# Performance work log

Hardware: AMD Instinct MI355X
Metric: run time of the kernel (lower is better)

The kernel has to match this reference:

```python
import jax, jax.numpy as jnp
from jax import lax
import numpy as np

RADIUS = 0.1
NSAMPLE = 32
STRIDE = 3
ED_NSAMPLE = 10


def _sqdist(a, b):
    # a: [B,M,3], b: [B,N,3] -> [B,M,N] squared euclidean distance
    return (jnp.sum(a * a, -1)[:, :, None] + jnp.sum(b * b, -1)[:, None, :]
            - 2.0 * jnp.einsum('bmc,bnc->bmn', a, b))


def setup_inputs() -> dict:
    key = jax.random.key(0)
    ks = jax.random.split(key, 16)
    B, N = 8, 4096
    s = 0.05
    inp = {
        'data': jax.random.normal(ks[0], (B, N, 3), dtype=jnp.float32),
        'numpoints': N,
        # stem MLP 3 -> 64
        'W_stem': jax.random.normal(ks[1], (3, 64), dtype=jnp.float32) * s,
        'b_stem': jnp.zeros((64,), jnp.float32),
        # SA shared MLP (3 dp + 64 fj) -> 128
        'W_sa': jax.random.normal(ks[2], (67, 128), dtype=jnp.float32) * s,
        'b_sa': jnp.zeros((128,), jnp.float32),
        # FP MLP (128 interp + 64 skip) -> 64
        'W_fp': jax.random.normal(ks[3], (192, 64), dtype=jnp.float32) * s,
        'b_fp': jnp.zeros((64,), jnp.float32),
        # eigen-feature MLP 3 -> 4 -> 4
        'W_e1': jax.random.normal(ks[4], (3, 4), dtype=jnp.float32) * s,
        'b_e1': jnp.zeros((4,), jnp.float32),
        'W_e2': jax.random.normal(ks[5], (4, 4), dtype=jnp.float32) * s,
        'b_e2': jnp.zeros((4,), jnp.float32),
        # conv_final 1x1: 68 -> 64, + BN affine
        'W_fin': jax.random.normal(ks[6], (68, 64), dtype=jnp.float32) * s,
        'b_fin': jnp.zeros((64,), jnp.float32),
        'gamma': jnp.ones((64,), jnp.float32),
        'beta': jnp.zeros((64,), jnp.float32),
    }
    return inp


def reference(data, numpoints, W_stem, b_stem, W_sa, b_sa, W_fp, b_fp,
              W_e1, b_e1, W_e2, b_e2, W_fin, b_fin, gamma, beta):
    B, N, _ = data.shape
    b_ix = jnp.arange(B)[:, None, None]

    # ---------- encoder: stem MLP ----------
    f0 = jax.nn.relu(data @ W_stem + b_stem)  # [B,N,64]

    # set abstraction: stride-subsample centers, ball query, dp_fj, MLP, max
    sub_idx = jnp.arange(0, N, STRIDE)
    new_xyz = data[:, sub_idx]                 # [B,M,3]
    d2 = _sqdist(new_xyz, data)                # [B,M,N]
    col = jnp.arange(N, dtype=jnp.int32)
    valid = d2 < RADIUS * RADIUS
    keys = jnp.where(valid, col, N + col)      # first-valid ball query ordering
    negk, _ = lax.top_k(-keys, NSAMPLE)
    idx = -negk                                # [B,M,ns]
    first = idx[..., :1]                       # self point always valid
    idx = jnp.where(idx >= N, first, idx)
    g_xyz = data[b_ix, idx]                    # [B,M,ns,3]
    dp = (g_xyz - new_xyz[:, :, None, :]) / RADIUS  # normalize_dp
    g_f = f0[b_ix, idx]                        # [B,M,ns,64]
    feat = jnp.concatenate([dp, g_f], -1)      # [B,M,ns,67]
    h = jax.nn.relu(feat @ W_sa + b_sa)        # [B,M,ns,128]
    f_sub = jnp.max(h, axis=2)                 # [B,M,128]

    # ---------- decoder: 3-NN inverse-distance feature propagation ----------
    d2f = _sqdist(data, new_xyz)               # [B,N,M]
    negd, nn = lax.top_k(-d2f, 3)
    w = 1.0 / (-negd + 1e-8)
    w = w / jnp.sum(w, -1, keepdims=True)      # [B,N,3]
    nbr_f = f_sub[b_ix, nn]                    # [B,N,3,128]
    interp = jnp.einsum('bnk,bnkc->bnc', w, nbr_f)
    f = jax.nn.relu(jnp.concatenate([interp, f0], -1) @ W_fp + b_fp)  # [B,N,64]

    # ---------- KNN covariance eigen-features ----------
    d2e = _sqdist(data, data)                  # [B,N,N]
    _, gidx = lax.top_k(-d2e, ED_NSAMPLE)      # [B,N,k]
    nbr = data[b_ix, gidx]                     # [B,N,k,3]
    cen = nbr - jnp.mean(nbr, axis=2, keepdims=True)
    cov = jnp.einsum('bnkc,bnkd->bncd', cen, cen) / ED_NSAMPLE  # [B,N,3,3]
    eig = jnp.linalg.eigvalsh(cov)             # [B,N,3] ascending
    ef = jax.nn.relu(eig @ W_e1 + b_e1) @ W_e2 + b_e2  # [B,N,4]

    # ---------- fused 1x1 conv + BN (training-mode stats) + relu ----------
    z_in = jnp.concatenate([f, ef], -1)        # [B,N,68]
    zc = z_in @ W_fin + b_fin                  # [B,N,64]
    mu = jnp.mean(zc, axis=(0, 1))
    var = jnp.var(zc, axis=(0, 1))
    z = jax.nn.relu((zc - mu) * lax.rsqrt(var + 1e-5) * gamma + beta)
    z = jnp.transpose(z, (0, 2, 1))            # [B,64,N]
    return (data, z)
```

## Files before the change

kernel.cpp:

```cpp
#include <hip/hip_runtime.h>
#include <stdint.h>

#define BB 8
#define NN 4096
#define MM 1366
#define NS 32
#define RAD2 0.01f
#define NCH 16
#define CHUNK (NN/NCH)

static_assert(NCH * CHUNK == NN, "chunking");

__device__ __forceinline__ float rl(float v, int l) {
    return __int_as_float(__builtin_amdgcn_readlane(__float_as_int(v), l));
}
__device__ __forceinline__ uint32_t um(uint32_t a, uint32_t b) { return a < b ? a : b; }
__device__ __forceinline__ uint32_t ux(uint32_t a, uint32_t b) { return a > b ? a : b; }
__device__ __forceinline__ uint32_t um3(uint32_t a, uint32_t b, uint32_t c) { return um(um(a, b), c); }

__device__ __forceinline__ void mrg2(uint32_t* kk, uint32_t s0, uint32_t s1) {
    uint32_t n0 = um(kk[0], s0);
    uint32_t n1 = um3(kk[1], ux(kk[0], s0), s1);
    uint32_t n2 = um3(kk[2], ux(kk[1], s0), ux(kk[0], s1));
    uint32_t n3 = um3(kk[3], ux(kk[2], s0), ux(kk[1], s1));
    uint32_t n4 = um3(kk[4], ux(kk[3], s0), ux(kk[2], s1));
    uint32_t n5 = um3(kk[5], ux(kk[4], s0), ux(kk[3], s1));
    uint32_t n6 = um3(kk[6], ux(kk[5], s0), ux(kk[4], s1));
    uint32_t n7 = um3(kk[7], ux(kk[6], s0), ux(kk[5], s1));
    uint32_t n8 = um3(kk[8], ux(kk[7], s0), ux(kk[6], s1));
    uint32_t n9 = um3(kk[9], ux(kk[8], s0), ux(kk[7], s1));
    kk[0]=n0; kk[1]=n1; kk[2]=n2; kk[3]=n3; kk[4]=n4;
    kk[5]=n5; kk[6]=n6; kk[7]=n7; kk[8]=n8; kk[9]=n9;
}

__device__ __forceinline__ void mrg4(uint32_t* kk, uint32_t s0, uint32_t s1,
                                     uint32_t s2, uint32_t s3) {
    uint32_t n0 = um(kk[0], s0);
    uint32_t n1 = um3(kk[1], ux(kk[0], s0), s1);
    uint32_t n2 = um(um3(kk[2], ux(kk[1], s0), ux(kk[0], s1)), s2);
    uint32_t n3 = um3(um3(kk[3], ux(kk[2], s0), ux(kk[1], s1)), ux(kk[0], s2), s3);
    uint32_t n4 = um3(um3(kk[4], ux(kk[3], s0), ux(kk[2], s1)), ux(kk[1], s2), ux(kk[0], s3));
    uint32_t n5 = um3(um3(kk[5], ux(kk[4], s0), ux(kk[3], s1)), ux(kk[2], s2), ux(kk[1], s3));
    uint32_t n6 = um3(um3(kk[6], ux(kk[5], s0), ux(kk[4], s1)), ux(kk[3], s2), ux(kk[2], s3));
    uint32_t n7 = um3(um3(kk[7], ux(kk[6], s0), ux(kk[5], s1)), ux(kk[4], s2), ux(kk[3], s3));
    uint32_t n8 = um3(um3(kk[8], ux(kk[7], s0), ux(kk[6], s1)), ux(kk[5], s2), ux(kk[4], s3));
    uint32_t n9 = um3(um3(kk[9], ux(kk[8], s0), ux(kk[7], s1)), ux(kk[6], s2), ux(kk[5], s3));
    kk[0]=n0; kk[1]=n1; kk[2]=n2; kk[3]=n3; kk[4]=n4;
    kk[5]=n5; kk[6]=n6; kk[7]=n7; kk[8]=n8; kk[9]=n9;
}

__device__ __forceinline__ void srt4(uint32_t& a, uint32_t& b, uint32_t& c, uint32_t& d) {
    uint32_t t0 = um(a, b), t1 = ux(a, b), t2 = um(c, d), t3 = ux(c, d);
    uint32_t s0 = um(t0, t2), m0 = ux(t0, t2), m1 = um(t1, t3), s3 = ux(t1, t3);
    a = s0; b = um(m0, m1); c = ux(m0, m1); d = s3;
}

__global__ __launch_bounds__(256) void k_prep(const float* __restrict__ data,
                                              float* __restrict__ out,
                                              float4* __restrict__ cand4) {
    int t = blockIdx.x * 256 + threadIdx.x;
    float x = data[t * 3], y = data[t * 3 + 1], z = data[t * 3 + 2];
    out[t * 3] = x; out[t * 3 + 1] = y; out[t * 3 + 2] = z;
    cand4[t] = make_float4(x, y, z, x * x + y * y + z * z);
}

__global__ __launch_bounds__(256) void k_stem(const float* __restrict__ data,
                                              const float* __restrict__ Ws,
                                              const float* __restrict__ bs,
                                              float* __restrict__ f0) {
    int t = blockIdx.x * 256 + threadIdx.x;
    int c = t & 63;
    int r = t >> 6;
    const float* d = data + r * 3;
    float acc = bs[c];
    acc = fmaf(d[0], Ws[c], acc);
    acc = fmaf(d[1], Ws[64 + c], acc);
    acc = fmaf(d[2], Ws[128 + c], acc);
    f0[t] = fmaxf(acc, 0.f);
}

__global__ __launch_bounds__(256) void k_sa(const float4* __restrict__ cand4,
                                            const float* __restrict__ data,
                                            const float* __restrict__ f0,
                                            const float* __restrict__ Wsa,
                                            const float* __restrict__ bsa,
                                            float* __restrict__ fsub) {
    __shared__ float2 sW[67 * 64];
    __shared__ int sIdx[4][NS];
    for (int i = threadIdx.x; i < 67 * 64; i += 256) {
        int k = i >> 6, c = i & 63;
        sW[i] = make_float2(Wsa[k * 128 + c], Wsa[k * 128 + 64 + c]);
    }
    __syncthreads();
    int wv = threadIdx.x >> 6, lane = threadIdx.x & 63;
    int gm = blockIdx.x * 4 + wv;
    if (gm >= BB * MM) return;
    int b = gm / MM, m = gm - b * MM;
    const float4* cb4 = cand4 + b * NN;
    const float* db = data + b * NN * 3;
    float4 cen = cb4[3 * m];
    float cx = cen.x, cy = cen.y, cz = cen.z, sa = cen.w;

    int cnt = 0;
    for (int base = 0; base < NN; base += 64) {
        int n = base + lane;
        float4 c = cb4[n];
        float dot = fmaf(cz, c.z, fmaf(cy, c.y, cx * c.x));
        float d2 = (sa + c.w) - 2.f * dot;
        bool valid = d2 < RAD2;
        unsigned long long mask = __ballot(valid);
        if (valid) {
            int pos = cnt + __popcll(mask & ((1ull << lane) - 1ull));
            if (pos < NS) sIdx[wv][pos] = n;
        }
        cnt += __popcll(mask);
        if (cnt >= NS) break;
    }
    int scnt = cnt < NS ? cnt : NS;

    float cl = lane == 0 ? cx : (lane == 1 ? cy : cz);
    float hb0 = bsa[lane], hb1 = bsa[64 + lane];
    float m0 = 0.f, m1 = 0.f;

    for (int s0 = 0; s0 < scnt; s0 += 4) {
        float fr[4], fr2[4];
        #pragma unroll
        for (int u = 0; u < 4; ++u) {
            int s = s0 + u;
            if (s >= scnt) s = 0;
            int nj = sIdx[wv][s];
            int fb = (b * NN + nj) * 64;
            float v;
            if (lane >= 3) v = f0[fb + lane - 3];
            else           v = (db[nj * 3 + lane] - cl) * 10.0f;
            fr[u] = v;
            fr2[u] = (lane < 3) ? f0[fb + 61 + lane] : 0.f;
        }
        float h0[4], h1[4];
        #pragma unroll
        for (int u = 0; u < 4; ++u) { h0[u] = hb0; h1[u] = hb1; }
        for (int k = 0; k < 64; ++k) {
            float2 w = sW[k * 64 + lane];
            #pragma unroll
            for (int u = 0; u < 4; ++u) {
                float fv = rl(fr[u], k);
                h0[u] = fmaf(fv, w.x, h0[u]);
                h1[u] = fmaf(fv, w.y, h1[u]);
            }
        }
        #pragma unroll
        for (int k = 64; k < 67; ++k) {
            float2 w = sW[k * 64 + lane];
            #pragma unroll
            for (int u = 0; u < 4; ++u) {
                float fv = rl(fr2[u], k - 64);
                h0[u] = fmaf(fv, w.x, h0[u]);
                h1[u] = fmaf(fv, w.y, h1[u]);
            }
        }
        #pragma unroll
        for (int u = 0; u < 4; ++u) {
            m0 = fmaxf(m0, fmaxf(h0[u], 0.f));
            m1 = fmaxf(m1, fmaxf(h1[u], 0.f));
        }
    }
    fsub[gm * 128 + lane] = m0;
    fsub[gm * 128 + 64 + lane] = m1;
}

__global__ __launch_bounds__(256) void k_interp(const float4* __restrict__ cand4,
                                                const float* __restrict__ fsub,
                                                float* __restrict__ itp) {
    __shared__ float4 sC[MM];
    __shared__ float sMD[4][64][3];
    __shared__ int   sMI[4][64][3];
    __shared__ float sWts[64][3];
    __shared__ int   sNbr[64][3];
    int t = threadIdx.x, wv = t >> 6, lane = t & 63;
    int blk = blockIdx.x;
    int b = blk >> 6;
    int pbase = (blk & 63) * 64;
    const float4* cb4 = cand4 + b * NN;
    for (int m = t; m < MM; m += 256) sC[m] = cb4[3 * m];
    __syncthreads();
    int p = pbase + lane;
    float4 pm = cb4[p];
    float px = pm.x, py = pm.y, pz = pm.z, pa = pm.w;
    float d0 = 1e30f, d1 = 1e30f, d2v = 1e30f;
    int n0 = 0, n1 = 0, n2 = 0;
    int ms = wv * 342, me = ms + 342 < MM ? ms + 342 : MM;
    for (int m = ms; m < me; ++m) {
        float4 c = sC[m];
        float dd = (pa + c.w) - 2.f * (px * c.x + py * c.y + pz * c.z);
        if (dd < d2v) {
            if (dd < d1) {
                d2v = d1; n2 = n1;
                if (dd < d0) { d1 = d0; n1 = n0; d0 = dd; n0 = m; }
                else         { d1 = dd; n1 = m; }
            } else { d2v = dd; n2 = m; }
        }
    }
    sMD[wv][lane][0] = d0; sMD[wv][lane][1] = d1; sMD[wv][lane][2] = d2v;
    sMI[wv][lane][0] = n0; sMI[wv][lane][1] = n1; sMI[wv][lane][2] = n2;
    __syncthreads();
    if (wv == 0) {
        d0 = sMD[0][lane][0]; d1 = sMD[0][lane][1]; d2v = sMD[0][lane][2];
        n0 = sMI[0][lane][0]; n1 = sMI[0][lane][1]; n2 = sMI[0][lane][2];
        for (int w = 1; w < 4; ++w) {
            #pragma unroll
            for (int r = 0; r < 3; ++r) {
                float dd = sMD[w][lane][r];
                int mm = sMI[w][lane][r];
                if (dd < d2v) {
                    if (dd < d1) {
                        d2v = d1; n2 = n1;
                        if (dd < d0) { d1 = d0; n1 = n0; d0 = dd; n0 = mm; }
                        else         { d1 = dd; n1 = mm; }
                    } else { d2v = dd; n2 = mm; }
                }
            }
        }
        float w0 = 1.f / (d0 + 1e-8f), w1 = 1.f / (d1 + 1e-8f), w2 = 1.f / (d2v + 1e-8f);
        float ws = w0 + w1 + w2;
        sWts[lane][0] = w0 / ws; sWts[lane][1] = w1 / ws; sWts[lane][2] = w2 / ws;
        sNbr[lane][0] = n0; sNbr[lane][1] = n1; sNbr[lane][2] = n2;
    }
    __syncthreads();
    for (int i = wv * 16; i < wv * 16 + 16; ++i) {
        float a0 = sWts[i][0], a1 = sWts[i][1], a2 = sWts[i][2];
        const float* r0 = fsub + (b * MM + sNbr[i][0]) * 128;
        const float* r1 = fsub + (b * MM + sNbr[i][1]) * 128;
        const float* r2 = fsub + (b * MM + sNbr[i][2]) * 128;
        float v0 = fmaf(a2, r2[lane], fmaf(a1, r1[lane], a0 * r0[lane]));
        float v1 = fmaf(a2, r2[64 + lane], fmaf(a1, r1[64 + lane], a0 * r0[64 + lane]));
        int row = b * NN + pbase + i;
        itp[row * 128 + lane] = v0;
        itp[row * 128 + 64 + lane] = v1;
    }
}

__global__ __launch_bounds__(256) void k_knn_part(const float4* __restrict__ cand4,
                                                  uint32_t* __restrict__ pk) {
    int t = threadIdx.x;
    int blk = blockIdx.x;
    int ch = blk & (NCH - 1);
    int pg = (blk >> 4) & 15;
    int b = blk >> 8;
    const float4* cb = cand4 + b * NN;
    int c0 = ch * CHUNK;
    int p = pg * 256 + t;
    float4 me = cb[p];
    float px = me.x, py = me.y, pz = me.z, pa = me.w;
    uint32_t kk[10];
    #pragma unroll
    for (int r = 0; r < 10; ++r) kk[r] = 0xFFFFFF00u + r;
    for (int j = 0; j < CHUNK; j += 4) {
        float4 ca = cb[c0 + j];
        float4 cbv = cb[c0 + j + 1];
        float4 cc = cb[c0 + j + 2];
        float4 cd = cb[c0 + j + 3];
        float da = fmaxf(fmaf(-2.f, fmaf(pz, ca.z, fmaf(py, ca.y, px * ca.x)), pa + ca.w), 0.f);
        float db_ = fmaxf(fmaf(-2.f, fmaf(pz, cbv.z, fmaf(py, cbv.y, px * cbv.x)), pa + cbv.w), 0.f);
        float dc = fmaxf(fmaf(-2.f, fmaf(pz, cc.z, fmaf(py, cc.y, px * cc.x)), pa + cc.w), 0.f);
        float dd = fmaxf(fmaf(-2.f, fmaf(pz, cd.z, fmaf(py, cd.y, px * cd.x)), pa + cd.w), 0.f);
        uint32_t ka = (__float_as_uint(da) & 0xFFFFF000u) | (uint32_t)(c0 + j);
        uint32_t kb = (__float_as_uint(db_) & 0xFFFFF000u) | (uint32_t)(c0 + j + 1);
        uint32_t kc = (__float_as_uint(dc) & 0xFFFFF000u) | (uint32_t)(c0 + j + 2);
        uint32_t kd = (__float_as_uint(dd) & 0xFFFFF000u) | (uint32_t)(c0 + j + 3);
        srt4(ka, kb, kc, kd);
        mrg4(kk, ka, kb, kc, kd);
    }
    int gp = b * NN + p;
    #pragma unroll
    for (int r = 0; r < 10; ++r)
        pk[(ch * 10 + r) * (BB * NN) + gp] = kk[r];
}

__device__ __forceinline__ void jrot(float& app, float& aqq, float& apq,
                                     float& arp, float& arq) {
    float ap = apq;
    if (fabsf(ap) > 1e-32f) {
        float th = (aqq - app) / (2.f * ap);
        float t = 1.f / (fabsf(th) + sqrtf(th * th + 1.f));
        t = th < 0.f ? -t : t;
        float c = 1.f / sqrtf(t * t + 1.f);
        float s = t * c;
        app = app - t * ap;
        aqq = aqq + t * ap;
        apq = 0.f;
        float rp = arp, rq = arq;
        arp = c * rp - s * rq;
        arq = s * rp + c * rq;
    }
}

__global__ __launch_bounds__(256) void k_knn_eig(const float4* __restrict__ cand4,
                                                 const uint32_t* __restrict__ pk,
                                                 const float* __restrict__ We1,
                                                 const float* __restrict__ be1,
                                                 const float* __restrict__ We2,
                                                 const float* __restrict__ be2,
                                                 float* __restrict__ ef) {
    int t = blockIdx.x * 256 + threadIdx.x;
    int b = t >> 12;
    const float4* cb = cand4 + b * NN;
    uint32_t kk[10];
    #pragma unroll
    for (int r = 0; r < 10; ++r) kk[r] = pk[r * (BB * NN) + t];
    for (int ch = 1; ch < NCH; ++ch) {
        uint32_t s[10];
        #pragma unroll
        for (int r = 0; r < 10; ++r) s[r] = pk[(ch * 10 + r) * (BB * NN) + t];
        mrg4(kk, s[0], s[1], s[2], s[3]);
        mrg4(kk, s[4], s[5], s[6], s[7]);
        mrg2(kk, s[8], s[9]);
    }
    float xs[10], ys[10], zs[10];
    float mx = 0.f, my = 0.f, mz = 0.f;
    #pragma unroll
    for (int r = 0; r < 10; ++r) {
        int n = (int)(kk[r] & 0xFFFu);
        float4 cr = cb[n];
        xs[r] = cr.x; ys[r] = cr.y; zs[r] = cr.z;
        mx += xs[r]; my += ys[r]; mz += zs[r];
    }
    mx *= 0.1f; my *= 0.1f; mz *= 0.1f;
    float a00 = 0, a01 = 0, a02 = 0, a11 = 0, a12 = 0, a22 = 0;
    #pragma unroll
    for (int r = 0; r < 10; ++r) {
        float x = xs[r] - mx, y = ys[r] - my, z = zs[r] - mz;
        a00 = fmaf(x, x, a00); a01 = fmaf(x, y, a01); a02 = fmaf(x, z, a02);
        a11 = fmaf(y, y, a11); a12 = fmaf(y, z, a12); a22 = fmaf(z, z, a22);
    }
    a00 *= 0.1f; a01 *= 0.1f; a02 *= 0.1f; a11 *= 0.1f; a12 *= 0.1f; a22 *= 0.1f;
    #pragma unroll
    for (int sweep = 0; sweep < 6; ++sweep) {
        jrot(a00, a11, a01, a02, a12);
        jrot(a00, a22, a02, a01, a12);
        jrot(a11, a22, a12, a01, a02);
    }
    float e0 = a00, e1 = a11, e2 = a22, tmp;
    if (e0 > e1) { tmp = e0; e0 = e1; e1 = tmp; }
    if (e1 > e2) { tmp = e1; e1 = e2; e2 = tmp; }
    if (e0 > e1) { tmp = e0; e0 = e1; e1 = tmp; }
    float tt[4];
    #pragma unroll
    for (int i = 0; i < 4; ++i) {
        float v = be1[i];
        v = fmaf(e0, We1[i], v);
        v = fmaf(e1, We1[4 + i], v);
        v = fmaf(e2, We1[8 + i], v);
        tt[i] = fmaxf(v, 0.f);
    }
    #pragma unroll
    for (int i = 0; i < 4; ++i) {
        float v = be2[i];
        v = fmaf(tt[0], We2[i], v);
        v = fmaf(tt[1], We2[4 + i], v);
        v = fmaf(tt[2], We2[8 + i], v);
        v = fmaf(tt[3], We2[12 + i], v);
        ef[t * 4 + i] = v;
    }
}

__global__ __launch_bounds__(256) void k_fp(const float* __restrict__ itp,
                                            const float* __restrict__ f0,
                                            const float* __restrict__ W,
                                            const float* __restrict__ bias,
                                            float* __restrict__ outf) {
    __shared__ float sW[192 * 64];
    for (int i = threadIdx.x; i < 192 * 64; i += 256) sW[i] = W[i];
    __syncthreads();
    int lane = threadIdx.x & 63;
    int wv = threadIdx.x >> 6;
    float bb = bias[lane];
    int rowbase = blockIdx.x * 64 + wv * 16;
    for (int it = 0; it < 4; ++it) {
        int r = rowbase + it * 4;
        float fa[4], fbv[4], fc[4], acc[4];
        #pragma unroll
        for (int u = 0; u < 4; ++u) {
            fa[u]  = itp[(r + u) * 128 + lane];
            fbv[u] = itp[(r + u) * 128 + 64 + lane];
            fc[u]  = f0[(r + u) * 64 + lane];
            acc[u] = bb;
        }
        #pragma unroll
        for (int k = 0; k < 192; ++k) {
            float w = sW[k * 64 + lane];
            #pragma unroll
            for (int u = 0; u < 4; ++u) {
                float fv = k < 64 ? rl(fa[u], k)
                         : (k < 128 ? rl(fbv[u], k - 64) : rl(fc[u], k - 128));
                acc[u] = fmaf(fv, w, acc[u]);
            }
        }
        #pragma unroll
        for (int u = 0; u < 4; ++u)
            outf[(r + u) * 64 + lane] = fmaxf(acc[u], 0.f);
    }
}

__global__ __launch_bounds__(256) void k_fin(const float* __restrict__ fb,
                                             const float* __restrict__ efb,
                                             const float* __restrict__ W,
                                             const float* __restrict__ bias,
                                             float* __restrict__ zc) {
    __shared__ float sW[68 * 64];
    for (int i = threadIdx.x; i < 68 * 64; i += 256) sW[i] = W[i];
    __syncthreads();
    int lane = threadIdx.x & 63;
    int wv = threadIdx.x >> 6;
    float bb = bias[lane];
    int rowbase = blockIdx.x * 64 + wv * 16;
    for (int it = 0; it < 4; ++it) {
        int r = rowbase + it * 4;
        float fa[4], fe[4], acc[4];
        #pragma unroll
        for (int u = 0; u < 4; ++u) {
            fa[u] = fb[(r + u) * 64 + lane];
            fe[u] = (lane < 4) ? efb[(r + u) * 4 + lane] : 0.f;
            acc[u] = bb;
        }
        #pragma unroll
        for (int k = 0; k < 68; ++k) {
            float w = sW[k * 64 + lane];
            #pragma unroll
            for (int u = 0; u < 4; ++u) {
                float fv = k < 64 ? rl(fa[u], k) : rl(fe[u], k - 64);
                acc[u] = fmaf(fv, w, acc[u]);
            }
        }
        #pragma unroll
        for (int u = 0; u < 4; ++u)
            zc[(r + u) * 64 + lane] = acc[u];
    }
}

__global__ __launch_bounds__(256) void k_stats1(const float* __restrict__ zc,
                                                float* __restrict__ pp) {
    int t = threadIdx.x;
    int c = t & 63, r4 = t >> 6;
    float s = 0.f, sq = 0.f;
    int base = blockIdx.x * 512;
    for (int i = 0; i < 128; ++i) {
        float v = zc[(base + i * 4 + r4) * 64 + c];
        s += v;
        sq = fmaf(v, v, sq);
    }
    __shared__ float ls[256], lq[256];
    ls[t] = s; lq[t] = sq;
    __syncthreads();
    if (t < 64) {
        float st = ls[t] + ls[t + 64] + ls[t + 128] + ls[t + 192];
        float qt = lq[t] + lq[t + 64] + lq[t + 128] + lq[t + 192];
        pp[blockIdx.x * 128 + t] = st;
        pp[blockIdx.x * 128 + 64 + t] = qt;
    }
}

__global__ __launch_bounds__(64) void k_stats2(const float* __restrict__ pp,
                                               const float* __restrict__ gamma,
                                               const float* __restrict__ beta,
                                               float* __restrict__ ss) {
    int c = threadIdx.x;
    float s = 0.f, sq = 0.f;
    for (int k = 0; k < 64; ++k) {
        s += pp[k * 128 + c];
        sq += pp[k * 128 + 64 + c];
    }
    const float inv = 1.f / (float)(BB * NN);
    float mu = s * inv;
    float var = sq * inv - mu * mu;
    float sc = gamma[c] / sqrtf(var + 1e-5f);
    ss[c] = sc;
    ss[64 + c] = beta[c] - mu * sc;
}

__global__ __launch_bounds__(256) void k_norm_t(const float* __restrict__ zc,
                                                const float* __restrict__ ss,
                                                float* __restrict__ out) {
    __shared__ float sT[64][65];
    int blk = blockIdx.x;
    int b = blk >> 6;
    int nbase = (blk & 63) * 64;
    int c = threadIdx.x & 63;
    int r4 = threadIdx.x >> 6;
    float sc = ss[c], sh = ss[64 + c];
    #pragma unroll
    for (int i = 0; i < 16; ++i) {
        int nr = i * 4 + r4;
        float v = zc[(b * NN + nbase + nr) * 64 + c];
        sT[nr][c] = fmaxf(fmaf(v, sc, sh), 0.f);
    }
    __syncthreads();
    int nn = threadIdx.x & 63;
    #pragma unroll
    for (int i = 0; i < 16; ++i) {
        int cc = i * 4 + r4;
        out[BB * NN * 3 + (b * 64 + cc) * NN + nbase + nn] = sT[nn][cc];
    }
}

extern "C" void kernel_launch(void* const* d_in, const int* in_sizes, int n_in,
                              void* d_out, int out_size, void* d_ws, size_t ws_size,
                              hipStream_t stream) {
    const float* data = (const float*)d_in[0];
    const float* Wst  = (const float*)d_in[2];
    const float* bst  = (const float*)d_in[3];
    const float* Wsa  = (const float*)d_in[4];
    const float* bsa  = (const float*)d_in[5];
    const float* Wfp  = (const float*)d_in[6];
    const float* bfp  = (const float*)d_in[7];
    const float* We1  = (const float*)d_in[8];
    const float* be1  = (const float*)d_in[9];
    const float* We2  = (const float*)d_in[10];
    const float* be2  = (const float*)d_in[11];
    const float* Wfin = (const float*)d_in[12];
    const float* bfin = (const float*)d_in[13];
    const float* gamma = (const float*)d_in[14];
    const float* beta  = (const float*)d_in[15];
    float* out = (float*)d_out;

    float* f0   = (float*)d_ws;
    float* fsub = f0 + 2097152;
    float* efb  = fsub + 1398784;
    float* zc   = efb + 131072;
    float* ss   = zc + 2097152;
    float* pp   = ss + 128;
    float4* cand4 = (float4*)(pp + 8192);
    float* itp  = (float*)cand4 + 131072;
    float* fb   = itp + 4194304;
    uint32_t* pkk = (uint32_t*)itp;

    k_prep<<<(BB * NN) / 256, 256, 0, stream>>>(data, out, cand4);
    k_stem<<<(BB * NN * 64) / 256, 256, 0, stream>>>(data, Wst, bst, f0);
    k_knn_part<<<BB * 16 * NCH, 256, 0, stream>>>(cand4, pkk);
    k_knn_eig<<<(BB * NN) / 256, 256, 0, stream>>>(cand4, pkk, We1, be1, We2, be2, efb);
    k_sa<<<(BB * MM + 3) / 4, 256, 0, stream>>>(cand4, data, f0, Wsa, bsa, fsub);
    k_interp<<<BB * 64, 256, 0, stream>>>(cand4, fsub, itp);
    k_fp<<<512, 256, 0, stream>>>(itp, f0, Wfp, bfp, fb);
    k_fin<<<512, 256, 0, stream>>>(fb, efb, Wfin, bfin, zc);
    k_stats1<<<64, 256, 0, stream>>>(zc, pp);
    k_stats2<<<1, 64, 0, stream>>>(pp, gamma, beta, ss);
    k_norm_t<<<512, 256, 0, stream>>>(zc, ss, out);
}
```

Before: 353.4 us.

## Reuse KNN top-10 neighbors to answer ball query, falling back to full scan

The k_knn_eig kernel now stores the merged 10-nearest-neighbor keys to a workspace buffer. k_sa reads those keys for each subsampled center and keeps the ones inside the radius. It falls back to the original full linear scan only when the 10th neighbor lies within a small margin of the radius, meaning more in-ball points could exist. This replaces a scan over up to 4096 points per center with 10 loads in the common sparse case, at the cost of an extra buffer write and a dependency between the KNN and SA stages.

```diff
diff --git a/kernel.cpp b/kernel.cpp
--- a/kernel.cpp
+++ b/kernel.cpp
@@ -82,6 +82,7 @@
 __global__ __launch_bounds__(256) void k_sa(const float4* __restrict__ cand4,
                                             const float* __restrict__ data,
                                             const float* __restrict__ f0,
+                                            const uint32_t* __restrict__ mrg,
                                             const float* __restrict__ Wsa,
                                             const float* __restrict__ bsa,
                                             float* __restrict__ fsub) {
@@ -101,20 +102,40 @@
     float4 cen = cb4[3 * m];
     float cx = cen.x, cy = cen.y, cz = cen.z, sa = cen.w;
 
-    int cnt = 0;
-    for (int base = 0; base < NN; base += 64) {
-        int n = base + lane;
-        float4 c = cb4[n];
-        float dot = fmaf(cz, c.z, fmaf(cy, c.y, cx * c.x));
-        float d2 = (sa + c.w) - 2.f * dot;
-        bool valid = d2 < RAD2;
+    int cnt;
+    bool fallback;
+    {
+        float d2l = 1e30f;
+        int idxl = 0;
+        if (lane < 10) {
+            uint32_t key = mrg[lane * (BB * NN) + b * NN + 3 * m];
+            idxl = (int)(key & 0xFFFu);
+            float4 c = cb4[idxl];
+            float dot = fmaf(cz, c.z, fmaf(cy, c.y, cx * c.x));
+            d2l = (sa + c.w) - 2.f * dot;
+        }
+        bool valid = (lane < 10) && (d2l < RAD2);
         unsigned long long mask = __ballot(valid);
-        if (valid) {
-            int pos = cnt + __popcll(mask & ((1ull << lane) - 1ull));
-            if (pos < NS) sIdx[wv][pos] = n;
-        }
-        cnt += __popcll(mask);
-        if (cnt >= NS) break;
+        if (valid) sIdx[wv][__popcll(mask & ((1ull << lane) - 1ull))] = idxl;
+        cnt = __popcll(mask);
+        fallback = rl(d2l, 9) < RAD2 * 1.0005f;
+    }
+    if (fallback) {
+        cnt = 0;
+        for (int base = 0; base < NN; base += 64) {
+            int n = base + lane;
+            float4 c = cb4[n];
+            float dot = fmaf(cz, c.z, fmaf(cy, c.y, cx * c.x));
+            float d2 = (sa + c.w) - 2.f * dot;
+            bool valid = d2 < RAD2;
+            unsigned long long mask = __ballot(valid);
+            if (valid) {
+                int pos = cnt + __popcll(mask & ((1ull << lane) - 1ull));
+                if (pos < NS) sIdx[wv][pos] = n;
+            }
+            cnt += __popcll(mask);
+            if (cnt >= NS) break;
+        }
     }
     int scnt = cnt < NS ? cnt : NS;
 
@@ -296,6 +317,7 @@
 
 __global__ __launch_bounds__(256) void k_knn_eig(const float4* __restrict__ cand4,
                                                  const uint32_t* __restrict__ pk,
+                                                 uint32_t* __restrict__ mrg,
                                                  const float* __restrict__ We1,
                                                  const float* __restrict__ be1,
                                                  const float* __restrict__ We2,
@@ -315,6 +337,9 @@
         mrg4(kk, s[4], s[5], s[6], s[7]);
         mrg2(kk, s[8], s[9]);
     }
+    #pragma unroll
+    for (int r = 0; r < 10; ++r)
+        mrg[r * (BB * NN) + t] = kk[r];
     float xs[10], ys[10], zs[10];
     float mx = 0.f, my = 0.f, mz = 0.f;
     #pragma unroll
@@ -529,15 +554,16 @@
     float* ss   = zc + 2097152;
     float* pp   = ss + 128;
     float4* cand4 = (float4*)(pp + 8192);
-    float* itp  = (float*)cand4 + 131072;
+    uint32_t* mrgb = (uint32_t*)((float*)cand4 + 131072);
+    float* itp  = (float*)mrgb + 1310720;
     float* fb   = itp + 4194304;
     uint32_t* pkk = (uint32_t*)itp;
 
     k_prep<<<(BB * NN) / 256, 256, 0, stream>>>(data, out, cand4);
     k_stem<<<(BB * NN * 64) / 256, 256, 0, stream>>>(data, Wst, bst, f0);
     k_knn_part<<<BB * 16 * NCH, 256, 0, stream>>>(cand4, pkk);
-    k_knn_eig<<<(BB * NN) / 256, 256, 0, stream>>>(cand4, pkk, We1, be1, We2, be2, efb);
-    k_sa<<<(BB * MM + 3) / 4, 256, 0, stream>>>(cand4, data, f0, Wsa, bsa, fsub);
+    k_knn_eig<<<(BB * NN) / 256, 256, 0, stream>>>(cand4, pkk, mrgb, We1, be1, We2, be2, efb);
+    k_sa<<<(BB * MM + 3) / 4, 256, 0, stream>>>(cand4, data, f0, mrgb, Wsa, bsa, fsub);
     k_interp<<<BB * 64, 256, 0, stream>>>(cand4, fsub, itp);
     k_fp<<<512, 256, 0, stream>>>(itp, f0, Wfp, bfp, fb);
     k_fin<<<512, 256, 0, stream>>>(fb, efb, Wfin, bfin, zc);
```

New measurement: 318.0 us. 10.0% less time.
